# Performance work log

Hardware: AMD Instinct MI355X
Metric: run time of the kernel (lower is better)

Reference implementation:

```python
import jax, jax.numpy as jnp
import numpy as np

SIZE = (160, 192, 160)  # matches init_kwargs `size`


def _make_grid(size):
    # torch: meshgrid(arange(s) for s, indexing='ij'), stack last dim, flip last dim
    vecs = [jnp.arange(s, dtype=jnp.float32) for s in size]
    g = jnp.stack(jnp.meshgrid(*vecs, indexing='ij'), axis=-1)
    g = g[..., ::-1]  # last-dim order becomes (x, y, z) = (W, H, D) indices
    return g[None]    # [1, D, H, W, 3]


def _grid_sample_3d(src, locs):
    """Trilinear grid_sample, align_corners=True, padding_mode='zeros'.
    src: [B, C, D, H, W]; locs: [B, D, H, W, 3] in [-1,1], last dim (x,y,z)."""
    B, C, D, H, W = src.shape
    dims_m1 = jnp.array([W - 1, H - 1, D - 1], jnp.float32)
    px = (locs + 1.0) * 0.5 * dims_m1  # unnormalize (align_corners=True)
    x, y, z = px[..., 0], px[..., 1], px[..., 2]
    x0 = jnp.floor(x); y0 = jnp.floor(y); z0 = jnp.floor(z)
    fx, fy, fz = x - x0, y - y0, z - z0
    x0i = x0.astype(jnp.int32); y0i = y0.astype(jnp.int32); z0i = z0.astype(jnp.int32)

    def gather(src_b, iz, iy, ix):  # src_b: [C,D,H,W]; idx: [D,H,W]
        return src_b[:, iz, iy, ix]  # [C,D,H,W]

    out = jnp.zeros(src.shape, src.dtype)
    for dz in (0, 1):
        for dy in (0, 1):
            for dx in (0, 1):
                ix, iy, iz = x0i + dx, y0i + dy, z0i + dz
                valid = (ix >= 0) & (ix < W) & (iy >= 0) & (iy < H) & (iz >= 0) & (iz < D)
                w = ((fx if dx else 1.0 - fx)
                     * (fy if dy else 1.0 - fy)
                     * (fz if dz else 1.0 - fz))
                w = jnp.where(valid, w, 0.0)  # zero padding for OOB
                icx = jnp.clip(ix, 0, W - 1)
                icy = jnp.clip(iy, 0, H - 1)
                icz = jnp.clip(iz, 0, D - 1)
                v = jax.vmap(gather)(src, icz, icy, icx)  # [B,C,D,H,W]
                out = out + w[:, None] * v
    return out


def setup_inputs() -> dict:
    key = jax.random.key(0)
    k1, k2 = jax.random.split(key)
    B, C = 2, 2
    D, H, W = SIZE
    src = jax.random.normal(k1, (B, C, D, H, W), dtype=jnp.float32)
    flow = jax.random.normal(k2, (B, 3, D, H, W), dtype=jnp.float32)
    return {"src": src, "flow": flow}


def reference(src, flow):
    # order='image': no flip of flow channels
    flow = jnp.moveaxis(flow, 1, -1)                      # [B,D,H,W,3]
    grid = _make_grid(SIZE)                                # [1,D,H,W,3]
    s = jnp.array(SIZE, jnp.float32)[::-1] - 1.0           # [W-1,H-1,D-1]
    new_locs = 2.0 * ((grid + flow) / s - 0.5)             # normalized [-1,1]
    return _grid_sample_3d(src, new_locs)
```

## Files before the change

kernel.cpp:

```cpp
#include <hip/hip_runtime.h>

#define DD 160
#define HH 192
#define WW 160
#define SP (DD * HH * WW)
#define NB 2
#define NC 2

#define TX 32
#define TY 8
#define TZ 8
#define RXW 40
#define RYH 15
#define RZD 15
#define REGC (RZD * RYH * RXW)
#define NCHUNK (REGC / 4)
#define NITER 5

#define NTX 5
#define NTY 24
#define NTZ 20
#define NTILES (NTX * NTY * NTZ * NB)
#define PER_XCD (NTILES / 8)

typedef float v2f __attribute__((ext_vector_type(2)));
typedef float v4f __attribute__((ext_vector_type(4)));

typedef const void __attribute__((address_space(1)))* gas_ptr;
typedef void __attribute__((address_space(3)))* las_ptr;

__device__ __forceinline__ void st4_nt(float* p, v4f v) {
    __builtin_nontemporal_store(v, reinterpret_cast<v4f*>(p));
}
__device__ __forceinline__ v2f ld2g(const float* p) {
    return *reinterpret_cast<const v2f*>(p);
}

__device__ __forceinline__ float sample_global1(
    const float* __restrict__ s,
    int x, int y, int z, float dx, float dy, float dz)
{
    float sx = (float)x + dx, sy = (float)y + dy, sz = (float)z + dz;
    float xf = floorf(sx), yf = floorf(sy), zf = floorf(sz);
    float fx = sx - xf, fy = sy - yf, fz = sz - zf;
    int x0 = (int)xf, y0 = (int)yf, z0 = (int)zf;
    int x1 = x0 + 1, y1 = y0 + 1, z1 = z0 + 1;

    float wx0 = (x0 >= 0 && x0 < WW) ? (1.0f - fx) : 0.0f;
    float wx1 = (x1 >= 0 && x1 < WW) ? fx : 0.0f;
    float wy0 = (y0 >= 0 && y0 < HH) ? (1.0f - fy) : 0.0f;
    float wy1 = (y1 >= 0 && y1 < HH) ? fy : 0.0f;
    float wz0 = (z0 >= 0 && z0 < DD) ? (1.0f - fz) : 0.0f;
    float wz1 = (z1 >= 0 && z1 < DD) ? fz : 0.0f;

    int p  = min(max(x0, 0), WW - 2);
    int i0 = min(max(x0, 0), WW - 1) - p;
    int i1 = min(max(x1, 0), WW - 1) - p;
    int cy0 = min(max(y0, 0), HH - 1), cy1 = min(max(y1, 0), HH - 1);
    int cz0 = min(max(z0, 0), DD - 1), cz1 = min(max(z1, 0), DD - 1);

    int o00 = (cz0 * HH + cy0) * WW + p;
    int o01 = (cz0 * HH + cy1) * WW + p;
    int o10 = (cz1 * HH + cy0) * WW + p;
    int o11 = (cz1 * HH + cy1) * WW + p;

    v2f c00 = ld2g(s + o00);
    v2f c01 = ld2g(s + o01);
    v2f c10 = ld2g(s + o10);
    v2f c11 = ld2g(s + o11);

    #define PICK(v, i) ((i) ? (v).y : (v).x)
    float r;
    r  = (wz0 * wy0) * (wx0 * PICK(c00, i0) + wx1 * PICK(c00, i1));
    r += (wz0 * wy1) * (wx0 * PICK(c01, i0) + wx1 * PICK(c01, i1));
    r += (wz1 * wy0) * (wx0 * PICK(c10, i0) + wx1 * PICK(c10, i1));
    r += (wz1 * wy1) * (wx0 * PICK(c11, i0) + wx1 * PICK(c11, i1));
    #undef PICK
    return r;
}

__device__ __forceinline__ void stage_channel(
    const float* __restrict__ cb, int X0, int Y0, int Z0, int tid, float* sbuf)
{
    #pragma unroll
    for (int i = 0; i < NITER; ++i) {
        int c = tid + i * 512;
        if (i < NITER - 1 || c < NCHUNK) {
            int lz  = c / 150;  int r2 = c - lz * 150;
            int ly  = r2 / 10;  int lxc = r2 - ly * 10;
            int mz = min(max(Z0 - 3 + lz, 0), DD - 1);
            int my = min(max(Y0 - 3 + ly, 0), HH - 1);
            int mx = min(max(X0 - 4 + lxc * 4, 0), WW - 4);
            const float* g = cb + (mz * HH + my) * WW + mx;
            __builtin_amdgcn_global_load_lds(
                (gas_ptr)g, (las_ptr)(sbuf + 4 * c), 16, 0, 0);
        }
    }
}

__device__ __forceinline__ void fix_edge(float* sbuf, int tid, bool left)
{
    if (tid < RZD * RYH) {
        int lz = tid / RYH, ly = tid - lz * RYH;
        int base = (lz * RYH + ly) * RXW + (left ? 0 : RXW - 4);
        if (left) {
            float v = sbuf[base];
            sbuf[base + 1] = v; sbuf[base + 2] = v; sbuf[base + 3] = v;
        } else {
            float v = sbuf[base + 3];
            sbuf[base] = v; sbuf[base + 1] = v; sbuf[base + 2] = v;
        }
    }
}

__device__ __forceinline__ float sample_lds(
    const float* __restrict__ sbuf,
    float lx, float ly, float lz, int rx0, int ry0, int rz0)
{
    float xf = floorf(lx), yf = floorf(ly), zf = floorf(lz);
    float fx = lx - xf, fy = ly - yf, fz = lz - zf;
    int ix = (int)xf, iy = (int)yf, iz = (int)zf;

    int vx0 = ix + rx0, vy0 = iy + ry0, vz0 = iz + rz0;
    float wx0 = (vx0 >= 0  && vx0 < WW)     ? (1.0f - fx) : 0.0f;
    float wx1 = (vx0 >= -1 && vx0 < WW - 1) ? fx          : 0.0f;
    float wy0 = (vy0 >= 0  && vy0 < HH)     ? (1.0f - fy) : 0.0f;
    float wy1 = (vy0 >= -1 && vy0 < HH - 1) ? fy          : 0.0f;
    float wz0 = (vz0 >= 0  && vz0 < DD)     ? (1.0f - fz) : 0.0f;
    float wz1 = (vz0 >= -1 && vz0 < DD - 1) ? fz          : 0.0f;

    const float* pB = sbuf + (iz * RYH + iy) * RXW + ix;
    float A00 = pB[0],        B00 = pB[1];
    float A01 = pB[RXW],      B01 = pB[RXW + 1];
    const float* pC = pB + RYH * RXW;
    float A10 = pC[0],        B10 = pC[1];
    float A11 = pC[RXW],      B11 = pC[RXW + 1];

    float c00 = wx0 * A00 + wx1 * B00;
    float c01 = wx0 * A01 + wx1 * B01;
    float c10 = wx0 * A10 + wx1 * B10;
    float c11 = wx0 * A11 + wx1 * B11;
    float m0  = wy0 * c00 + wy1 * c01;
    float m1  = wy0 * c10 + wy1 * c11;
    return wz0 * m0 + wz1 * m1;
}

__global__ __launch_bounds__(512, 8) void st_warp_kernel(
    const float* __restrict__ src,
    const float* __restrict__ flow,
    float* __restrict__ out)
{
    __shared__ float sbuf[REGC];

    int u   = blockIdx.x;
    int tl  = (u & 7) * PER_XCD + (u >> 3);
    int tx  = tl % NTX;  int t2 = tl / NTX;
    int ty  = t2 % NTY;  int t3 = t2 / NTY;
    int tz  = t3 % NTZ;  int b  = t3 / NTZ;
    int X0 = tx * TX, Y0 = ty * TY, Z0 = tz * TZ;
    int tid = threadIdx.x;

    const bool edge = (tx == 0) | (tx == NTX - 1);
    const bool left = (tx == 0);

    const float* sb = src + b * NC * SP;

    int rr = tid >> 3;
    int xi = (tid & 7) << 2;
    int yl = rr & 7, zl = rr >> 3;
    int y = Y0 + yl, z = Z0 + zl, x = X0 + xi;
    int go = (z * HH + y) * WW + x;
    const float* fp = flow + b * 3 * SP + go;
    float* op = out + b * NC * SP + go;
    const int rx0 = X0 - 4, ry0 = Y0 - 3, rz0 = Z0 - 3;

    stage_channel(sb, X0, Y0, Z0, tid, sbuf);

    {
        v4f dxv = *reinterpret_cast<const v4f*>(fp);
        v4f dyv = *reinterpret_cast<const v4f*>(fp + SP);
        v4f dzv = *reinterpret_cast<const v4f*>(fp + 2 * SP);

        __syncthreads();
        if (edge) {
            fix_edge(sbuf, tid, left);
            __syncthreads();
        }

        float a[4];
        #pragma unroll
        for (int j = 0; j < 4; ++j) {
            float dx = dxv[j], dy = dyv[j], dz = dzv[j];
            bool inH = (dx >= -4.0f) & (dx < 4.0f) &
                       (dy >= -3.0f) & (dy < 4.0f) &
                       (dz >= -3.0f) & (dz < 4.0f);
            if (inH) {
                float lx = (float)(xi + j + 4) + dx;
                float ly = (float)(yl + 3) + dy;
                float lz = (float)(zl + 3) + dz;
                a[j] = sample_lds(sbuf, lx, ly, lz, rx0, ry0, rz0);
            } else {
                a[j] = sample_global1(sb, x + j, y, z, dx, dy, dz);
            }
        }
        v4f o = {a[0], a[1], a[2], a[3]};
        st4_nt(op, o);
    }
    __syncthreads();

    stage_channel(sb + SP, X0, Y0, Z0, tid, sbuf);

    {
        v4f dxv = *reinterpret_cast<const v4f*>(fp);
        v4f dyv = *reinterpret_cast<const v4f*>(fp + SP);
        v4f dzv = *reinterpret_cast<const v4f*>(fp + 2 * SP);

        __syncthreads();
        if (edge) {
            fix_edge(sbuf, tid, left);
            __syncthreads();
        }

        float a[4];
        #pragma unroll
        for (int j = 0; j < 4; ++j) {
            float dx = dxv[j], dy = dyv[j], dz = dzv[j];
            bool inH = (dx >= -4.0f) & (dx < 4.0f) &
                       (dy >= -3.0f) & (dy < 4.0f) &
                       (dz >= -3.0f) & (dz < 4.0f);
            if (inH) {
                float lx = (float)(xi + j + 4) + dx;
                float ly = (float)(yl + 3) + dy;
                float lz = (float)(zl + 3) + dz;
                a[j] = sample_lds(sbuf, lx, ly, lz, rx0, ry0, rz0);
            } else {
                a[j] = sample_global1(sb + SP, x + j, y, z, dx, dy, dz);
            }
        }
        v4f o = {a[0], a[1], a[2], a[3]};
        st4_nt(op + SP, o);
    }
}

extern "C" void kernel_launch(void* const* d_in, const int* in_sizes, int n_in,
                              void* d_out, int out_size, void* d_ws, size_t ws_size,
                              hipStream_t stream) {
    const float* src  = (const float*)d_in[0];
    const float* flow = (const float*)d_in[1];
    float* out = (float*)d_out;

    st_warp_kernel<<<NTILES, 512, 0, stream>>>(src, flow, out);
}
```

Baseline: 283.3 us.

## Convert warp kernel to persistent double-buffered LDS pipeline across tiles

The kernel becomes persistent: 512 blocks each walk a strided list of tiles within their XCD partition. Two LDS buffers let channel 1's halo stage while channel 0 is computed, and the next tile's channel 0 plus its flow vectors are prefetched while channel 1 is computed. This is meant to hide global-to-LDS load latency and cut per-block launch and sync overhead. The edge-fixup pass and its extra barrier are removed, since the replicated halo cells only ever get zero weights, and flow loads become nontemporal. In exchange, LDS per block doubles and launch bounds drop, which lowers occupancy, and the final iteration's tile tail may be unbalanced.

```diff
diff --git a/kernel.cpp b/kernel.cpp
--- a/kernel.cpp
+++ b/kernel.cpp
@@ -21,7 +21,8 @@
 #define NTY 24
 #define NTZ 20
 #define NTILES (NTX * NTY * NTZ * NB)
-#define PER_XCD (NTILES / 8)
+#define TPX (NTILES / 8)
+#define NBLK 512
 
 typedef float v2f __attribute__((ext_vector_type(2)));
 typedef float v4f __attribute__((ext_vector_type(4)));
@@ -29,6 +30,9 @@
 typedef const void __attribute__((address_space(1)))* gas_ptr;
 typedef void __attribute__((address_space(3)))* las_ptr;
 
+__device__ __forceinline__ v4f ld4_nt(const float* p) {
+    return __builtin_nontemporal_load(reinterpret_cast<const v4f*>(p));
+}
 __device__ __forceinline__ void st4_nt(float* p, v4f v) {
     __builtin_nontemporal_store(v, reinterpret_cast<v4f*>(p));
 }
@@ -98,21 +102,6 @@
     }
 }
 
-__device__ __forceinline__ void fix_edge(float* sbuf, int tid, bool left)
-{
-    if (tid < RZD * RYH) {
-        int lz = tid / RYH, ly = tid - lz * RYH;
-        int base = (lz * RYH + ly) * RXW + (left ? 0 : RXW - 4);
-        if (left) {
-            float v = sbuf[base];
-            sbuf[base + 1] = v; sbuf[base + 2] = v; sbuf[base + 3] = v;
-        } else {
-            float v = sbuf[base + 3];
-            sbuf[base] = v; sbuf[base + 1] = v; sbuf[base + 2] = v;
-        }
-    }
-}
-
 __device__ __forceinline__ float sample_lds(
     const float* __restrict__ sbuf,
     float lx, float ly, float lz, int rx0, int ry0, int rz0)
@@ -145,100 +134,103 @@
     return wz0 * m0 + wz1 * m1;
 }
 
-__global__ __launch_bounds__(512, 8) void st_warp_kernel(
+struct Geo {
+    int X0, Y0, Z0;
+    int x, y, z;
+    const float* sb;
+    const float* fp;
+    float* op;
+};
+
+__device__ __forceinline__ Geo decode_tile(
+    int tl, const float* src, const float* flow, float* out,
+    int xi, int yl, int zl)
+{
+    Geo g;
+    int tx = tl % NTX;  int t2 = tl / NTX;
+    int ty = t2 % NTY;  int t3 = t2 / NTY;
+    int tz = t3 % NTZ;  int b  = t3 / NTZ;
+    g.X0 = tx * TX; g.Y0 = ty * TY; g.Z0 = tz * TZ;
+    g.x = g.X0 + xi; g.y = g.Y0 + yl; g.z = g.Z0 + zl;
+    int go = (g.z * HH + g.y) * WW + g.x;
+    g.sb = src + b * NC * SP;
+    g.fp = flow + b * 3 * SP + go;
+    g.op = out + b * NC * SP + go;
+    return g;
+}
+
+__device__ __forceinline__ void compute_store(
+    const float* __restrict__ sbuf, const Geo& g, int cofs,
+    v4f dxv, v4f dyv, v4f dzv, int xi, int yl, int zl)
+{
+    const int rx0 = g.X0 - 4, ry0 = g.Y0 - 3, rz0 = g.Z0 - 3;
+    float a[4];
+    #pragma unroll
+    for (int j = 0; j < 4; ++j) {
+        float dx = dxv[j], dy = dyv[j], dz = dzv[j];
+        bool inH = (dx >= -4.0f) & (dx < 4.0f) &
+                   (dy >= -3.0f) & (dy < 4.0f) &
+                   (dz >= -3.0f) & (dz < 4.0f);
+        if (inH) {
+            float lx = (float)(xi + j + 4) + dx;
+            float ly = (float)(yl + 3) + dy;
+            float lz = (float)(zl + 3) + dz;
+            a[j] = sample_lds(sbuf, lx, ly, lz, rx0, ry0, rz0);
+        } else {
+            a[j] = sample_global1(g.sb + cofs, g.x + j, g.y, g.z, dx, dy, dz);
+        }
+    }
+    v4f o = {a[0], a[1], a[2], a[3]};
+    st4_nt(g.op + cofs, o);
+}
+
+__global__ __launch_bounds__(512, 4) void st_warp_kernel(
     const float* __restrict__ src,
     const float* __restrict__ flow,
     float* __restrict__ out)
 {
-    __shared__ float sbuf[REGC];
-
-    int u   = blockIdx.x;
-    int tl  = (u & 7) * PER_XCD + (u >> 3);
-    int tx  = tl % NTX;  int t2 = tl / NTX;
-    int ty  = t2 % NTY;  int t3 = t2 / NTY;
-    int tz  = t3 % NTZ;  int b  = t3 / NTZ;
-    int X0 = tx * TX, Y0 = ty * TY, Z0 = tz * TZ;
-    int tid = threadIdx.x;
-
-    const bool edge = (tx == 0) | (tx == NTX - 1);
-    const bool left = (tx == 0);
-
-    const float* sb = src + b * NC * SP;
+    __shared__ float sA[REGC];
+    __shared__ float sB[REGC];
+
+    int u    = blockIdx.x;
+    int xcd  = u & 7;
+    int slot = u >> 3;
+    int tid  = threadIdx.x;
 
     int rr = tid >> 3;
     int xi = (tid & 7) << 2;
     int yl = rr & 7, zl = rr >> 3;
-    int y = Y0 + yl, z = Z0 + zl, x = X0 + xi;
-    int go = (z * HH + y) * WW + x;
-    const float* fp = flow + b * 3 * SP + go;
-    float* op = out + b * NC * SP + go;
-    const int rx0 = X0 - 4, ry0 = Y0 - 3, rz0 = Z0 - 3;
-
-    stage_channel(sb, X0, Y0, Z0, tid, sbuf);
-
-    {
-        v4f dxv = *reinterpret_cast<const v4f*>(fp);
-        v4f dyv = *reinterpret_cast<const v4f*>(fp + SP);
-        v4f dzv = *reinterpret_cast<const v4f*>(fp + 2 * SP);
-
+
+    int nt = (TPX - slot + 63) >> 6;
+    int tl = xcd * TPX + slot;
+
+    Geo g = decode_tile(tl, src, flow, out, xi, yl, zl);
+    stage_channel(g.sb, g.X0, g.Y0, g.Z0, tid, sA);
+    v4f dxv = ld4_nt(g.fp);
+    v4f dyv = ld4_nt(g.fp + SP);
+    v4f dzv = ld4_nt(g.fp + 2 * SP);
+
+    for (int t = 0; t < nt; ++t) {
         __syncthreads();
-        if (edge) {
-            fix_edge(sbuf, tid, left);
-            __syncthreads();
+
+        stage_channel(g.sb + SP, g.X0, g.Y0, g.Z0, tid, sB);
+        compute_store(sA, g, 0, dxv, dyv, dzv, xi, yl, zl);
+
+        __syncthreads();
+
+        bool more = (t + 1 < nt);
+        Geo gn = g;
+        v4f nxv = dxv, nyv = dyv, nzv = dzv;
+        if (more) {
+            gn = decode_tile(tl + ((t + 1) << 6), src, flow, out, xi, yl, zl);
+            stage_channel(gn.sb, gn.X0, gn.Y0, gn.Z0, tid, sA);
+            nxv = ld4_nt(gn.fp);
+            nyv = ld4_nt(gn.fp + SP);
+            nzv = ld4_nt(gn.fp + 2 * SP);
         }
-
-        float a[4];
-        #pragma unroll
-        for (int j = 0; j < 4; ++j) {
-            float dx = dxv[j], dy = dyv[j], dz = dzv[j];
-            bool inH = (dx >= -4.0f) & (dx < 4.0f) &
-                       (dy >= -3.0f) & (dy < 4.0f) &
-                       (dz >= -3.0f) & (dz < 4.0f);
-            if (inH) {
-                float lx = (float)(xi + j + 4) + dx;
-                float ly = (float)(yl + 3) + dy;
-                float lz = (float)(zl + 3) + dz;
-                a[j] = sample_lds(sbuf, lx, ly, lz, rx0, ry0, rz0);
-            } else {
-                a[j] = sample_global1(sb, x + j, y, z, dx, dy, dz);
-            }
-        }
-        v4f o = {a[0], a[1], a[2], a[3]};
-        st4_nt(op, o);
-    }
-    __syncthreads();
-
-    stage_channel(sb + SP, X0, Y0, Z0, tid, sbuf);
-
-    {
-        v4f dxv = *reinterpret_cast<const v4f*>(fp);
-        v4f dyv = *reinterpret_cast<const v4f*>(fp + SP);
-        v4f dzv = *reinterpret_cast<const v4f*>(fp + 2 * SP);
-
-        __syncthreads();
-        if (edge) {
-            fix_edge(sbuf, tid, left);
-            __syncthreads();
-        }
-
-        float a[4];
-        #pragma unroll
-        for (int j = 0; j < 4; ++j) {
-            float dx = dxv[j], dy = dyv[j], dz = dzv[j];
-            bool inH = (dx >= -4.0f) & (dx < 4.0f) &
-                       (dy >= -3.0f) & (dy < 4.0f) &
-                       (dz >= -3.0f) & (dz < 4.0f);
-            if (inH) {
-                float lx = (float)(xi + j + 4) + dx;
-                float ly = (float)(yl + 3) + dy;
-                float lz = (float)(zl + 3) + dz;
-                a[j] = sample_lds(sbuf, lx, ly, lz, rx0, ry0, rz0);
-            } else {
-                a[j] = sample_global1(sb + SP, x + j, y, z, dx, dy, dz);
-            }
-        }
-        v4f o = {a[0], a[1], a[2], a[3]};
-        st4_nt(op + SP, o);
+        compute_store(sB, g, SP, dxv, dyv, dzv, xi, yl, zl);
+
+        g = gn; dxv = nxv; dyv = nyv; dzv = nzv;
     }
 }
 
@@ -249,5 +241,5 @@
     const float* flow = (const float*)d_in[1];
     float* out = (float*)d_out;
 
-    st_warp_kernel<<<NTILES, 512, 0, stream>>>(src, flow, out);
-}
+    st_warp_kernel<<<NBLK, 512, 0, stream>>>(src, flow, out);
+}
```

Result: faster. 269.2 us (-5.0%).
